# Kernel optimization log

Hardware: AMD Instinct MI355X
Metric: run time of the kernel (lower is better)

## Reference

```python
import jax, jax.numpy as jnp
import numpy as np
from jax import lax

SLOPE = 5.0        # ProbMask slope
BIN_SLOPE = 10.0   # Binarize backward slope
SPARSITY = 8192.0 / 65536.0  # budget / input_size = 0.125
BATCH, N = 512, 65536


def setup_inputs() -> dict:
    key = jax.random.key(0)
    kx, kw = jax.random.split(key)
    x = jax.random.normal(kx, (BATCH, N), dtype=jnp.float32)
    # ProbMask._generate_logits: uniform in (eps, 1-eps), inverse-sigmoid / slope
    eps = 0.01
    u = jax.random.uniform(kw, (N,), dtype=jnp.float32, minval=eps, maxval=1.0 - eps)
    weights = -jnp.log(1.0 / u - 1.0) / SLOPE
    return {"x": x, "weights": weights}


def _sample_u(p):
    """Rejection-sample uniform u until mean(u <= p) is within 10% of SPARSITY.
    Device-resident lax.while_loop replacing the host-sync Python loop."""
    def draw(k):
        k, sub = jax.random.split(k)
        return k, jax.random.uniform(sub, p.shape, dtype=p.dtype)

    def cond(carry):
        _, u = carry
        m = jnp.mean((u <= p).astype(jnp.float32))
        return jnp.abs(m - SPARSITY) / SPARSITY > 0.1

    def body(carry):
        k, _ = carry
        return draw(k)

    carry0 = draw(jax.random.key(42))
    _, u = lax.while_loop(cond, body, carry0)
    return u


def binarize(p):
    u = _sample_u(p)
    return (u <= p).astype(p.dtype)


def reference(x, weights):
    # ProbMask: broadcast weights over batch, sigmoid(slope * logits)
    prob = jax.nn.sigmoid(SLOPE * (0.0 * x[..., 0:1] + weights))  # [B, N]
    # RescaleProbMap: force mean toward SPARSITY
    xbar = jnp.mean(prob)
    r = SPARSITY / xbar
    beta = (1.0 - SPARSITY) / (1.0 - xbar)
    le = (r <= 1.0).astype(prob.dtype)
    rescaled = le * prob * r + (1.0 - le) * (1.0 - (1.0 - prob) * beta)
    # Binarize via rejection-sampled uniform threshold
    mask = binarize(rescaled)
    return mask * x
```

## Files before the change

kernel.cpp:

```cpp
#include <hip/hip_runtime.h>
#include <stdint.h>

#define ROT(x, r) (((x) << (r)) | ((x) >> (32 - (r))))

__device__ __forceinline__ void tf_block(uint32_t k0, uint32_t k1,
                                         uint32_t x0, uint32_t x1,
                                         uint32_t& o0, uint32_t& o1) {
  uint32_t ks2 = k0 ^ k1 ^ 0x1BD11BDAu;
  x0 += k0; x1 += k1;
  x0 += x1; x1 = ROT(x1,13); x1 ^= x0;
  x0 += x1; x1 = ROT(x1,15); x1 ^= x0;
  x0 += x1; x1 = ROT(x1,26); x1 ^= x0;
  x0 += x1; x1 = ROT(x1, 6); x1 ^= x0;
  x0 += k1; x1 += ks2 + 1u;
  x0 += x1; x1 = ROT(x1,17); x1 ^= x0;
  x0 += x1; x1 = ROT(x1,29); x1 ^= x0;
  x0 += x1; x1 = ROT(x1,16); x1 ^= x0;
  x0 += x1; x1 = ROT(x1,24); x1 ^= x0;
  x0 += ks2; x1 += k0 + 2u;
  x0 += x1; x1 = ROT(x1,13); x1 ^= x0;
  x0 += x1; x1 = ROT(x1,15); x1 ^= x0;
  x0 += x1; x1 = ROT(x1,26); x1 ^= x0;
  x0 += x1; x1 = ROT(x1, 6); x1 ^= x0;
  x0 += k0; x1 += k1 + 3u;
  x0 += x1; x1 = ROT(x1,17); x1 ^= x0;
  x0 += x1; x1 = ROT(x1,29); x1 ^= x0;
  x0 += x1; x1 = ROT(x1,16); x1 ^= x0;
  x0 += x1; x1 = ROT(x1,24); x1 ^= x0;
  x0 += k1; x1 += ks2 + 4u;
  x0 += x1; x1 = ROT(x1,13); x1 ^= x0;
  x0 += x1; x1 = ROT(x1,15); x1 ^= x0;
  x0 += x1; x1 = ROT(x1,26); x1 ^= x0;
  x0 += x1; x1 = ROT(x1, 6); x1 ^= x0;
  o0 = x0 + ks2;
  o1 = x1 + k0 + 5u;
}

__device__ inline float xla_tanh_f32(float x) {
#pragma clang fp contract(off)
  float ax = fabsf(x);
  float xc = fminf(fmaxf(x, -9.0f), 9.0f);
  float x2 = xc * xc;
  float num = -2.76076847742355e-16f;
  num = x2 * num + 2.00018790482477e-13f;
  num = x2 * num + -8.60467152213735e-11f;
  num = x2 * num + 5.12229709037114e-08f;
  num = x2 * num + 1.48572235717979e-05f;
  num = x2 * num + 6.37261928875436e-04f;
  num = x2 * num + 4.89352455891786e-03f;
  num = xc * num;
  float den = 1.19825839466702e-06f;
  den = x2 * den + 1.18534705686654e-04f;
  den = x2 * den + 2.26843463243900e-03f;
  den = x2 * den + 4.89352518554385e-03f;
  float res = num / den;
  return (ax < 0.0004f) ? x : res;
}

__device__ inline float sigmoid_xla(float s) {
#pragma clang fp contract(off)
  float t = xla_tanh_f32(0.5f * s);
  return 0.5f + 0.5f * t;
}

__global__ void prob_kernel(const float* __restrict__ w, float* __restrict__ prob) {
#pragma clang fp contract(off)
  int n = blockIdx.x * 256 + threadIdx.x;
  float s = 5.0f * w[n];
  prob[n] = sigmoid_xla(s);
}

__global__ void rowsum_thresh_kernel(const float* __restrict__ prob,
                                     uint32_t* __restrict__ thresh) {
#pragma clang fp contract(off)
  __shared__ double sm[256];
  __shared__ float sv[3];
  double acc = 0.0;
  for (int j = 0; j < 256; ++j) acc += (double)prob[j * 256 + threadIdx.x];
  sm[threadIdx.x] = acc;
  __syncthreads();
  for (int off = 128; off > 0; off >>= 1) {
    if (threadIdx.x < off) sm[threadIdx.x] += sm[threadIdx.x + off];
    __syncthreads();
  }
  if (threadIdx.x == 0) {
    double S = sm[0];
    float xbar = (float)(S / 65536.0);
    float r    = 0.125f / xbar;
    float beta = 0.875f / (1.0f - xbar);
    sv[0] = r; sv[1] = beta; sv[2] = (r <= 1.0f) ? 1.0f : 0.0f;
  }
  __syncthreads();
  float r = sv[0], beta = sv[1], le = sv[2];
  for (int j = 0; j < 256; ++j) {
    int n = j * 256 + threadIdx.x;
    float p = prob[n];
    float resc = (le != 0.0f) ? (p * r) : (1.0f - (1.0f - p) * beta);
    double f = floor((double)resc * 8388608.0);
    if (f > 8388607.0) f = 8388607.0;
    thresh[n] = (uint32_t)f;
  }
}

__global__ __launch_bounds__(256) void mask_kernel(
    const float4* __restrict__ x4, const uint32_t* __restrict__ thresh,
    float4* __restrict__ out4, uint32_t sk0, uint32_t sk1) {
  uint32_t t  = blockIdx.x * 256u + threadIdx.x;
  uint32_t i0 = t * 8u;
  uint32_t n0 = i0 & 65535u;
  const uint4* tp = reinterpret_cast<const uint4*>(thresh + n0);
  uint4 Ta = tp[0];
  uint4 Tb = tp[1];
  float4 xa = x4[2u * t];
  float4 xb = x4[2u * t + 1u];
  uint32_t m[8];
#pragma unroll
  for (int j = 0; j < 8; ++j) {
    uint32_t o0, o1;
    tf_block(sk0, sk1, 0u, i0 + (uint32_t)j, o0, o1);
    m[j] = (o0 ^ o1) >> 9;
  }
  float4 oa, ob;
  oa.x = (m[0] <= Ta.x) ? xa.x : 0.0f;
  oa.y = (m[1] <= Ta.y) ? xa.y : 0.0f;
  oa.z = (m[2] <= Ta.z) ? xa.z : 0.0f;
  oa.w = (m[3] <= Ta.w) ? xa.w : 0.0f;
  ob.x = (m[4] <= Tb.x) ? xb.x : 0.0f;
  ob.y = (m[5] <= Tb.y) ? xb.y : 0.0f;
  ob.z = (m[6] <= Tb.z) ? xb.z : 0.0f;
  ob.w = (m[7] <= Tb.w) ? xb.w : 0.0f;
  out4[2u * t]      = oa;
  out4[2u * t + 1u] = ob;
}

extern "C" void kernel_launch(void* const* d_in, const int* in_sizes, int n_in,
                              void* d_out, int out_size, void* d_ws, size_t ws_size,
                              hipStream_t stream) {
  const float* x;
  const float* w;
  if (in_sizes[0] == 65536) { w = (const float*)d_in[0]; x = (const float*)d_in[1]; }
  else                      { x = (const float*)d_in[0]; w = (const float*)d_in[1]; }
  float* out = (float*)d_out;

  float*    prob   = (float*)d_ws;
  uint32_t* thresh = (uint32_t*)((char*)d_ws + 65536 * 4);

  uint32_t s0, s1;
  tf_block_host:;
  {
    uint32_t k0 = 0u, k1 = 42u, x0 = 0u, x1 = 1u;
    uint32_t ks2 = k0 ^ k1 ^ 0x1BD11BDAu;
    x0 += k0; x1 += k1;
    x0 += x1; x1 = ROT(x1,13); x1 ^= x0;
    x0 += x1; x1 = ROT(x1,15); x1 ^= x0;
    x0 += x1; x1 = ROT(x1,26); x1 ^= x0;
    x0 += x1; x1 = ROT(x1, 6); x1 ^= x0;
    x0 += k1; x1 += ks2 + 1u;
    x0 += x1; x1 = ROT(x1,17); x1 ^= x0;
    x0 += x1; x1 = ROT(x1,29); x1 ^= x0;
    x0 += x1; x1 = ROT(x1,16); x1 ^= x0;
    x0 += x1; x1 = ROT(x1,24); x1 ^= x0;
    x0 += ks2; x1 += k0 + 2u;
    x0 += x1; x1 = ROT(x1,13); x1 ^= x0;
    x0 += x1; x1 = ROT(x1,15); x1 ^= x0;
    x0 += x1; x1 = ROT(x1,26); x1 ^= x0;
    x0 += x1; x1 = ROT(x1, 6); x1 ^= x0;
    x0 += k0; x1 += k1 + 3u;
    x0 += x1; x1 = ROT(x1,17); x1 ^= x0;
    x0 += x1; x1 = ROT(x1,29); x1 ^= x0;
    x0 += x1; x1 = ROT(x1,16); x1 ^= x0;
    x0 += x1; x1 = ROT(x1,24); x1 ^= x0;
    x0 += k1; x1 += ks2 + 4u;
    x0 += x1; x1 = ROT(x1,13); x1 ^= x0;
    x0 += x1; x1 = ROT(x1,15); x1 ^= x0;
    x0 += x1; x1 = ROT(x1,26); x1 ^= x0;
    x0 += x1; x1 = ROT(x1, 6); x1 ^= x0;
    s0 = x0 + ks2;
    s1 = x1 + k0 + 5u;
  }

  prob_kernel<<<256, 256, 0, stream>>>(w, prob);
  rowsum_thresh_kernel<<<1, 256, 0, stream>>>(prob, thresh);
  mask_kernel<<<16384, 256, 0, stream>>>((const float4*)x, thresh, (float4*)out, s0, s1);
}
```

Before: 90.98 us.

## Parallelize probability reduction and threshold computation across many blocks

```diff
diff --git a/kernel.cpp b/kernel.cpp
--- a/kernel.cpp
+++ b/kernel.cpp
@@ -3,37 +3,42 @@
 
 #define ROT(x, r) (((x) << (r)) | ((x) >> (32 - (r))))
 
+#define TF_BODY(k0, k1, x0, x1, o0, o1)                                  \
+  {                                                                      \
+    uint32_t ks2 = (k0) ^ (k1) ^ 0x1BD11BDAu;                            \
+    x0 += (k0); x1 += (k1);                                              \
+    x0 += x1; x1 = ROT(x1,13); x1 ^= x0;                                 \
+    x0 += x1; x1 = ROT(x1,15); x1 ^= x0;                                 \
+    x0 += x1; x1 = ROT(x1,26); x1 ^= x0;                                 \
+    x0 += x1; x1 = ROT(x1, 6); x1 ^= x0;                                 \
+    x0 += (k1); x1 += ks2 + 1u;                                          \
+    x0 += x1; x1 = ROT(x1,17); x1 ^= x0;                                 \
+    x0 += x1; x1 = ROT(x1,29); x1 ^= x0;                                 \
+    x0 += x1; x1 = ROT(x1,16); x1 ^= x0;                                 \
+    x0 += x1; x1 = ROT(x1,24); x1 ^= x0;                                 \
+    x0 += ks2; x1 += (k0) + 2u;                                          \
+    x0 += x1; x1 = ROT(x1,13); x1 ^= x0;                                 \
+    x0 += x1; x1 = ROT(x1,15); x1 ^= x0;                                 \
+    x0 += x1; x1 = ROT(x1,26); x1 ^= x0;                                 \
+    x0 += x1; x1 = ROT(x1, 6); x1 ^= x0;                                 \
+    x0 += (k0); x1 += (k1) + 3u;                                         \
+    x0 += x1; x1 = ROT(x1,17); x1 ^= x0;                                 \
+    x0 += x1; x1 = ROT(x1,29); x1 ^= x0;                                 \
+    x0 += x1; x1 = ROT(x1,16); x1 ^= x0;                                 \
+    x0 += x1; x1 = ROT(x1,24); x1 ^= x0;                                 \
+    x0 += (k1); x1 += ks2 + 4u;                                          \
+    x0 += x1; x1 = ROT(x1,13); x1 ^= x0;                                 \
+    x0 += x1; x1 = ROT(x1,15); x1 ^= x0;                                 \
+    x0 += x1; x1 = ROT(x1,26); x1 ^= x0;                                 \
+    x0 += x1; x1 = ROT(x1, 6); x1 ^= x0;                                 \
+    o0 = x0 + ks2;                                                       \
+    o1 = x1 + (k0) + 5u;                                                 \
+  }
+
 __device__ __forceinline__ void tf_block(uint32_t k0, uint32_t k1,
                                          uint32_t x0, uint32_t x1,
                                          uint32_t& o0, uint32_t& o1) {
-  uint32_t ks2 = k0 ^ k1 ^ 0x1BD11BDAu;
-  x0 += k0; x1 += k1;
-  x0 += x1; x1 = ROT(x1,13); x1 ^= x0;
-  x0 += x1; x1 = ROT(x1,15); x1 ^= x0;
-  x0 += x1; x1 = ROT(x1,26); x1 ^= x0;
-  x0 += x1; x1 = ROT(x1, 6); x1 ^= x0;
-  x0 += k1; x1 += ks2 + 1u;
-  x0 += x1; x1 = ROT(x1,17); x1 ^= x0;
-  x0 += x1; x1 = ROT(x1,29); x1 ^= x0;
-  x0 += x1; x1 = ROT(x1,16); x1 ^= x0;
-  x0 += x1; x1 = ROT(x1,24); x1 ^= x0;
-  x0 += ks2; x1 += k0 + 2u;
-  x0 += x1; x1 = ROT(x1,13); x1 ^= x0;
-  x0 += x1; x1 = ROT(x1,15); x1 ^= x0;
-  x0 += x1; x1 = ROT(x1,26); x1 ^= x0;
-  x0 += x1; x1 = ROT(x1, 6); x1 ^= x0;
-  x0 += k0; x1 += k1 + 3u;
-  x0 += x1; x1 = ROT(x1,17); x1 ^= x0;
-  x0 += x1; x1 = ROT(x1,29); x1 ^= x0;
-  x0 += x1; x1 = ROT(x1,16); x1 ^= x0;
-  x0 += x1; x1 = ROT(x1,24); x1 ^= x0;
-  x0 += k1; x1 += ks2 + 4u;
-  x0 += x1; x1 = ROT(x1,13); x1 ^= x0;
-  x0 += x1; x1 = ROT(x1,15); x1 ^= x0;
-  x0 += x1; x1 = ROT(x1,26); x1 ^= x0;
-  x0 += x1; x1 = ROT(x1, 6); x1 ^= x0;
-  o0 = x0 + ks2;
-  o1 = x1 + k0 + 5u;
+  TF_BODY(k0, k1, x0, x1, o0, o1)
 }
 
 __device__ inline float xla_tanh_f32(float x) {
@@ -63,21 +68,27 @@
   return 0.5f + 0.5f * t;
 }
 
-__global__ void prob_kernel(const float* __restrict__ w, float* __restrict__ prob) {
+__global__ void prob_sum_kernel(const float* __restrict__ w, float* __restrict__ prob,
+                                double* __restrict__ partial) {
 #pragma clang fp contract(off)
+  __shared__ double sm[256];
   int n = blockIdx.x * 256 + threadIdx.x;
   float s = 5.0f * w[n];
-  prob[n] = sigmoid_xla(s);
+  float p = sigmoid_xla(s);
+  prob[n] = p;
+  sm[threadIdx.x] = (double)p;
+  __syncthreads();
+  for (int off = 128; off > 0; off >>= 1) {
+    if (threadIdx.x < off) sm[threadIdx.x] += sm[threadIdx.x + off];
+    __syncthreads();
+  }
+  if (threadIdx.x == 0) partial[blockIdx.x] = sm[0];
 }
 
-__global__ void rowsum_thresh_kernel(const float* __restrict__ prob,
-                                     uint32_t* __restrict__ thresh) {
+__global__ void final_kernel(const double* __restrict__ partial, float* __restrict__ sc) {
 #pragma clang fp contract(off)
   __shared__ double sm[256];
-  __shared__ float sv[3];
-  double acc = 0.0;
-  for (int j = 0; j < 256; ++j) acc += (double)prob[j * 256 + threadIdx.x];
-  sm[threadIdx.x] = acc;
+  sm[threadIdx.x] = partial[threadIdx.x];
   __syncthreads();
   for (int off = 128; off > 0; off >>= 1) {
     if (threadIdx.x < off) sm[threadIdx.x] += sm[threadIdx.x + off];
@@ -88,18 +99,21 @@
     float xbar = (float)(S / 65536.0);
     float r    = 0.125f / xbar;
     float beta = 0.875f / (1.0f - xbar);
-    sv[0] = r; sv[1] = beta; sv[2] = (r <= 1.0f) ? 1.0f : 0.0f;
+    sc[0] = r; sc[1] = beta; sc[2] = (r <= 1.0f) ? 1.0f : 0.0f;
   }
-  __syncthreads();
-  float r = sv[0], beta = sv[1], le = sv[2];
-  for (int j = 0; j < 256; ++j) {
-    int n = j * 256 + threadIdx.x;
-    float p = prob[n];
-    float resc = (le != 0.0f) ? (p * r) : (1.0f - (1.0f - p) * beta);
-    double f = floor((double)resc * 8388608.0);
-    if (f > 8388607.0) f = 8388607.0;
-    thresh[n] = (uint32_t)f;
-  }
+}
+
+__global__ void thresh_kernel(const float* __restrict__ prob,
+                              const float* __restrict__ sc,
+                              uint32_t* __restrict__ thresh) {
+#pragma clang fp contract(off)
+  int n = blockIdx.x * 256 + threadIdx.x;
+  float r = sc[0], beta = sc[1], le = sc[2];
+  float p = prob[n];
+  float resc = (le != 0.0f) ? (p * r) : (1.0f - (1.0f - p) * beta);
+  double f = floor((double)resc * 8388608.0);
+  if (f > 8388607.0) f = 8388607.0;
+  thresh[n] = (uint32_t)f;
 }
 
 __global__ __launch_bounds__(256) void mask_kernel(
@@ -142,44 +156,20 @@
   else                      { x = (const float*)d_in[0]; w = (const float*)d_in[1]; }
   float* out = (float*)d_out;
 
-  float*    prob   = (float*)d_ws;
-  uint32_t* thresh = (uint32_t*)((char*)d_ws + 65536 * 4);
+  float*    prob    = (float*)d_ws;
+  uint32_t* thresh  = (uint32_t*)((char*)d_ws + 65536 * 4);
+  double*   partial = (double*)((char*)d_ws + 2 * 65536 * 4);
+  float*    sc      = (float*)((char*)d_ws + 2 * 65536 * 4 + 2048);
 
   uint32_t s0, s1;
-  tf_block_host:;
   {
-    uint32_t k0 = 0u, k1 = 42u, x0 = 0u, x1 = 1u;
-    uint32_t ks2 = k0 ^ k1 ^ 0x1BD11BDAu;
-    x0 += k0; x1 += k1;
-    x0 += x1; x1 = ROT(x1,13); x1 ^= x0;
-    x0 += x1; x1 = ROT(x1,15); x1 ^= x0;
-    x0 += x1; x1 = ROT(x1,26); x1 ^= x0;
-    x0 += x1; x1 = ROT(x1, 6); x1 ^= x0;
-    x0 += k1; x1 += ks2 + 1u;
-    x0 += x1; x1 = ROT(x1,17); x1 ^= x0;
-    x0 += x1; x1 = ROT(x1,29); x1 ^= x0;
-    x0 += x1; x1 = ROT(x1,16); x1 ^= x0;
-    x0 += x1; x1 = ROT(x1,24); x1 ^= x0;
-    x0 += ks2; x1 += k0 + 2u;
-    x0 += x1; x1 = ROT(x1,13); x1 ^= x0;
-    x0 += x1; x1 = ROT(x1,15); x1 ^= x0;
-    x0 += x1; x1 = ROT(x1,26); x1 ^= x0;
-    x0 += x1; x1 = ROT(x1, 6); x1 ^= x0;
-    x0 += k0; x1 += k1 + 3u;
-    x0 += x1; x1 = ROT(x1,17); x1 ^= x0;
-    x0 += x1; x1 = ROT(x1,29); x1 ^= x0;
-    x0 += x1; x1 = ROT(x1,16); x1 ^= x0;
-    x0 += x1; x1 = ROT(x1,24); x1 ^= x0;
-    x0 += k1; x1 += ks2 + 4u;
-    x0 += x1; x1 = ROT(x1,13); x1 ^= x0;
-    x0 += x1; x1 = ROT(x1,15); x1 ^= x0;
-    x0 += x1; x1 = ROT(x1,26); x1 ^= x0;
-    x0 += x1; x1 = ROT(x1, 6); x1 ^= x0;
-    s0 = x0 + ks2;
-    s1 = x1 + k0 + 5u;
+    uint32_t k0 = 0u, k1 = 42u, x0 = 0u, x1 = 1u, o0, o1;
+    TF_BODY(k0, k1, x0, x1, o0, o1)
+    s0 = o0; s1 = o1;
   }
 
-  prob_kernel<<<256, 256, 0, stream>>>(w, prob);
-  rowsum_thresh_kernel<<<1, 256, 0, stream>>>(prob, thresh);
+  prob_sum_kernel<<<256, 256, 0, stream>>>(w, prob, partial);
+  final_kernel<<<1, 256, 0, stream>>>(partial, sc);
+  thresh_kernel<<<256, 256, 0, stream>>>(prob, sc, thresh);
   mask_kernel<<<16384, 256, 0, stream>>>((const float4*)x, thresh, (float4*)out, s0, s1);
 }
```

Measured after the change: 75.90 us. -16.6%, faster.
